# Optimization experiments

Hardware: AMD Instinct MI355X
Metric: run time of the kernel (lower is better)

## Reference

```python
import jax, jax.numpy as jnp
import numpy as np

N_NODES = 100000
N_EDGES = 1600000
IN_DIM = 64
HIDDEN = 64
N_CLASSES = 249


def sage_conv(x, edge_index, W_l, b_l, W_r):
    # PyG SAGEConv with aggr='add': out = lin_l(sum_{j->i} x_j) + lin_r(x_i)
    src, dst = edge_index[0], edge_index[1]
    msgs = x[src]                                   # [E, d] gather
    agg = jax.ops.segment_sum(msgs, dst, num_segments=x.shape[0])  # [N, d]
    return agg @ W_l.T + b_l + x @ W_r.T


def setup_inputs() -> dict:
    key = jax.random.key(0)
    ks = jax.random.split(key, 8)
    x = jax.random.normal(ks[0], (N_NODES, IN_DIM), dtype=jnp.float32)
    edge_index = jax.random.randint(ks[1], (2, N_EDGES), 0, N_NODES, dtype=jnp.int64 if jax.config.jax_enable_x64 else jnp.int32)
    s1 = 1.0 / np.sqrt(IN_DIM)
    s2 = 1.0 / np.sqrt(HIDDEN)
    W1_l = jax.random.uniform(ks[2], (HIDDEN, IN_DIM), jnp.float32, -s1, s1)
    b1_l = jax.random.uniform(ks[3], (HIDDEN,), jnp.float32, -s1, s1)
    W1_r = jax.random.uniform(ks[4], (HIDDEN, IN_DIM), jnp.float32, -s1, s1)
    W2_l = jax.random.uniform(ks[5], (N_CLASSES, HIDDEN), jnp.float32, -s2, s2)
    b2_l = jax.random.uniform(ks[6], (N_CLASSES,), jnp.float32, -s2, s2)
    W2_r = jax.random.uniform(ks[7], (N_CLASSES, HIDDEN), jnp.float32, -s2, s2)
    return {"x": x, "edge_index": edge_index, "W1_l": W1_l, "b1_l": b1_l,
            "W1_r": W1_r, "W2_l": W2_l, "b2_l": b2_l, "W2_r": W2_r}


def reference(x, edge_index, W1_l, b1_l, W1_r, W2_l, b2_l, W2_r):
    h = sage_conv(x, edge_index, W1_l, b1_l, W1_r)
    h = jax.nn.relu(h)
    # dropout p=0.5 is identity at inference (training=False)
    out = sage_conv(h, edge_index, W2_l, b2_l, W2_r)
    return out
```

## Files before the change

### kernel.cpp

```cpp
#include <hip/hip_runtime.h>

#define DIM 64
#define NCLS 249
#define SCAN_CHUNK 1024
#define NCHUNK 192
#define PSHIFT 7
#define PSIZE 128
#define SBITS 17
#define SMASK ((1u << SBITS) - 1)
#define MAXP 1024

typedef unsigned int u32;
typedef unsigned short u16;
using bf16x8 = __attribute__((ext_vector_type(8))) short;
using f32x4  = __attribute__((ext_vector_type(4))) float;

__device__ __forceinline__ u16 f2bf(float f) {
    u32 u = __builtin_bit_cast(u32, f);
    u += 0x7FFFu + ((u >> 16) & 1u);
    return (u16)(u >> 16);
}
__device__ __forceinline__ float bf_lo(u32 u) { return __builtin_bit_cast(float, u << 16); }
__device__ __forceinline__ float bf_hi(u32 u) { return __builtin_bit_cast(float, u & 0xFFFF0000u); }

__global__ __launch_bounds__(256) void bucket_count(const int* __restrict__ dst, int E,
                                                    int chunk_size, int nxp,
                                                    int* __restrict__ bcnt) {
    __shared__ int c[MAXP];
    int t = threadIdx.x;
    for (int i = t; i < nxp; i += 256) c[i] = 0;
    __syncthreads();
    int base = blockIdx.x * chunk_size;
    int end = min(base + chunk_size, E);
    for (int e = base + t; e < end; e += 256) {
        int d = __builtin_nontemporal_load(&dst[e]);
        atomicAdd(&c[d >> PSHIFT], 1);
    }
    __syncthreads();
    for (int i = t; i < nxp; i += 256) bcnt[i * NCHUNK + blockIdx.x] = c[i];
}

__global__ __launch_bounds__(256) void scan_block_sums(const int* __restrict__ cnt, int n,
                                                       int* __restrict__ bsum) {
    __shared__ int sdata[256];
    int b = blockIdx.x, t = threadIdx.x;
    int base = b * SCAN_CHUNK;
    int s = 0;
    for (int i = t; i < SCAN_CHUNK; i += 256) {
        int idx = base + i;
        s += (idx < n) ? cnt[idx] : 0;
    }
    sdata[t] = s;
    __syncthreads();
    for (int off = 128; off > 0; off >>= 1) {
        if (t < off) sdata[t] += sdata[t + off];
        __syncthreads();
    }
    if (t == 0) bsum[b] = sdata[0];
}

__global__ __launch_bounds__(1024) void scan_bsum(int* __restrict__ bsum, int nb) {
    __shared__ int tmp[1024];
    int t = threadIdx.x;
    int v = (t < nb) ? bsum[t] : 0;
    tmp[t] = v;
    __syncthreads();
    for (int off = 1; off < 1024; off <<= 1) {
        int u = (t >= off) ? tmp[t - off] : 0;
        __syncthreads();
        tmp[t] += u;
        __syncthreads();
    }
    if (t < nb) bsum[t] = tmp[t] - v;
}

__global__ __launch_bounds__(256) void scan_final_boff(const int* __restrict__ cnt, int n,
                                                       const int* __restrict__ bsum,
                                                       int* __restrict__ boff, int total) {
    __shared__ int tsum[256];
    int b = blockIdx.x, t = threadIdx.x;
    int base = b * SCAN_CHUNK + t * 4;
    int v[4];
    int s = 0;
#pragma unroll
    for (int i = 0; i < 4; ++i) {
        int id = base + i;
        v[i] = (id < n) ? cnt[id] : 0;
        s += v[i];
    }
    tsum[t] = s;
    __syncthreads();
    for (int off = 1; off < 256; off <<= 1) {
        int u = (t >= off) ? tsum[t - off] : 0;
        __syncthreads();
        tsum[t] += u;
        __syncthreads();
    }
    int run = tsum[t] - s + bsum[b];
#pragma unroll
    for (int i = 0; i < 4; ++i) {
        int id = base + i;
        if (id < n) boff[id] = run;
        run += v[i];
    }
    if (b == 0 && t == 0) boff[n] = total;
}

__global__ __launch_bounds__(256) void bucket_scatter(const int* __restrict__ ei, int E,
                                                      int chunk_size, int nxp,
                                                      const int* __restrict__ boff,
                                                      u32* __restrict__ bucket) {
    __shared__ int cur[MAXP];
    int t = threadIdx.x;
    for (int i = t; i < nxp; i += 256) cur[i] = boff[i * NCHUNK + blockIdx.x];
    __syncthreads();
    int base = blockIdx.x * chunk_size;
    int end = min(base + chunk_size, E);
    for (int e = base + t; e < end; e += 256) {
        int s = __builtin_nontemporal_load(&ei[e]);
        int d = __builtin_nontemporal_load(&ei[E + e]);
        int pos = atomicAdd(&cur[d >> PSHIFT], 1);
        bucket[pos] = ((u32)(d & (PSIZE - 1)) << SBITS) | (u32)s;
    }
}

__global__ __launch_bounds__(256) void sort_bucket(const u32* __restrict__ bucket,
                                                   const int* __restrict__ boff,
                                                   int* __restrict__ nbr,
                                                   int* __restrict__ row_ptr,
                                                   int n, int E) {
    __shared__ int cnt[PSIZE];
    __shared__ int sc[PSIZE];
    __shared__ int cur[PSIZE];
    int t = threadIdx.x;
    int p = blockIdx.x;
    if (t < PSIZE) cnt[t] = 0;
    __syncthreads();
    int beg = boff[p * NCHUNK];
    int end = boff[(p + 1) * NCHUNK];
    for (int i = beg + t; i < end; i += 256)
        atomicAdd(&cnt[bucket[i] >> SBITS], 1);
    __syncthreads();
    if (t < PSIZE) sc[t] = cnt[t];
    __syncthreads();
    for (int off = 1; off < PSIZE; off <<= 1) {
        int v = 0;
        if (t < PSIZE && t >= off) v = sc[t - off];
        __syncthreads();
        if (t < PSIZE) sc[t] += v;
        __syncthreads();
    }
    if (t < PSIZE) {
        int excl = beg + sc[t] - cnt[t];
        cur[t] = excl;
        int node = p * PSIZE + t;
        if (node < n) row_ptr[node] = excl;
    }
    if (p == 0 && t == 0) row_ptr[n] = E;
    __syncthreads();
    for (int i = beg + t; i < end; i += 256) {
        u32 pk = bucket[i];
        int pos = atomicAdd(&cur[pk >> SBITS], 1);
        nbr[pos] = (int)(pk & SMASK);
    }
}

__global__ void prep_all(const float* __restrict__ x, u16* __restrict__ A1, int nx8,
                         const float* __restrict__ W1l, const float* __restrict__ W1r,
                         u16* __restrict__ B1,
                         const float* __restrict__ W2l, const float* __restrict__ W2r,
                         u16* __restrict__ B2) {
    int i = blockIdx.x * 256 + threadIdx.x;
    if (i < nx8) {
        int node = i >> 3, seg = i & 7;
        const float4 v0 = *(const float4*)(x + (size_t)i * 8);
        const float4 v1 = *(const float4*)(x + (size_t)i * 8 + 4);
        uint4 o;
        o.x = (u32)f2bf(v0.x) | ((u32)f2bf(v0.y) << 16);
        o.y = (u32)f2bf(v0.z) | ((u32)f2bf(v0.w) << 16);
        o.z = (u32)f2bf(v1.x) | ((u32)f2bf(v1.y) << 16);
        o.w = (u32)f2bf(v1.z) | ((u32)f2bf(v1.w) << 16);
        *(uint4*)(A1 + (size_t)node * 128 + 64 + seg * 8) = o;
        return;
    }
    int j = i - nx8;
    if (j < 64 * 128) {
        int r = j >> 7, k = j & 127;
        B1[j] = f2bf(k < 64 ? W1l[r * 64 + k] : W1r[r * 64 + k - 64]);
        return;
    }
    j -= 64 * 128;
    if (j < 256 * 128) {
        int r = j >> 7, k = j & 127;
        float v = 0.f;
        if (r < NCLS) v = (k < 64) ? W2l[r * 64 + k] : W2r[r * 64 + k - 64];
        B2[j] = f2bf(v);
    }
}

__global__ __launch_bounds__(256) void pull_bf16(const u16* __restrict__ Asrc,
                                                 const int* __restrict__ row_ptr,
                                                 const int* __restrict__ nbr,
                                                 u16* __restrict__ Adst, int n) {
    int tid = blockIdx.x * 256 + threadIdx.x;
    int node = tid >> 3;
    int q = tid & 7;
    if (node >= n) return;
    int beg = row_ptr[node], end = row_ptr[node + 1];
    float a0 = 0.f, a1 = 0.f, a2 = 0.f, a3 = 0.f, a4 = 0.f, a5 = 0.f, a6 = 0.f, a7 = 0.f;
    for (int j0 = beg; j0 < end; j0 += 8) {
        int myj = j0 + q;
        int smine = (myj < end) ? nbr[myj] : 0;
        int cnt = min(8, end - j0);
#pragma unroll 4
        for (int k = 0; k < cnt; ++k) {
            int s = __shfl(smine, k, 8);
            uint4 v = *(const uint4*)(Asrc + (size_t)s * 128 + 64 + q * 8);
            a0 += bf_lo(v.x); a1 += bf_hi(v.x);
            a2 += bf_lo(v.y); a3 += bf_hi(v.y);
            a4 += bf_lo(v.z); a5 += bf_hi(v.z);
            a6 += bf_lo(v.w); a7 += bf_hi(v.w);
        }
    }
    uint4 o;
    o.x = (u32)f2bf(a0) | ((u32)f2bf(a1) << 16);
    o.y = (u32)f2bf(a2) | ((u32)f2bf(a3) << 16);
    o.z = (u32)f2bf(a4) | ((u32)f2bf(a5) << 16);
    o.w = (u32)f2bf(a6) | ((u32)f2bf(a7) << 16);
    *(uint4*)(Adst + (size_t)node * 128 + q * 8) = o;
}

template<int NT, bool RELU, bool OUT_BF16>
__global__ __launch_bounds__(256) void gemm_kernel(
    const u16* __restrict__ A, const u16* __restrict__ B,
    const float* __restrict__ bias,
    float* __restrict__ outf, u16* __restrict__ outb,
    int n_nodes, int n_cols)
{
    constexpr int KC = (NT == 16) ? 2 : 1;
    constexpr int KW = 128 / KC;
    constexpr int RG = KW / 8;
    constexpr int NR = NT * 16;
    __shared__ uint4 smem[3072];
    uint4* A_lds = smem;
    uint4* B_lds = smem + 1024;

    const int t = threadIdx.x;
    const int node0 = blockIdx.x * 64;

#pragma unroll
    for (int i = 0; i < 4; ++i) {
        int gl = t + 256 * i;
        int r = gl >> 4, g = gl & 15;
        uint4 v = make_uint4(0u, 0u, 0u, 0u);
        int node = node0 + r;
        if (node < n_nodes) v = *(const uint4*)(A + (size_t)node * 128 + g * 8);
        A_lds[r * 16 + (g ^ (r & 7))] = v;
    }

    const int w  = t >> 6;
    const int l  = t & 63;
    const int lm = l & 15;
    const int lg = l >> 4;
    const int arow = w * 16 + lm;
    const int asw  = arow & 7;

    f32x4 acc[NT];
#pragma unroll
    for (int n = 0; n < NT; ++n) acc[n] = f32x4{0.f, 0.f, 0.f, 0.f};

#pragma unroll
    for (int kc = 0; kc < KC; ++kc) {
        __syncthreads();
#pragma unroll
        for (int i = 0; i < (NR * RG) / 256; ++i) {
            int gl = t + 256 * i;
            int r = gl / RG, g = gl % RG;
            uint4 v = *(const uint4*)(B + (size_t)r * 128 + kc * KW + g * 8);
            B_lds[r * RG + (g ^ (r & 7))] = v;
        }
        __syncthreads();
#pragma unroll
        for (int ks = 0; ks < KW / 32; ++ks) {
            int ag = lg + (kc * (KW / 32) + ks) * 4;
            bf16x8 af = __builtin_bit_cast(bf16x8, A_lds[arow * 16 + (ag ^ asw)]);
#pragma unroll
            for (int n = 0; n < NT; ++n) {
                int brow = n * 16 + lm;
                int bg = lg + ks * 4;
                bf16x8 bf = __builtin_bit_cast(bf16x8, B_lds[brow * RG + (bg ^ (brow & 7))]);
                acc[n] = __builtin_amdgcn_mfma_f32_16x16x32_bf16(af, bf, acc[n], 0, 0, 0);
            }
        }
    }

    if (OUT_BF16) {
        const int rbase = w * 16 + lg * 4;
#pragma unroll
        for (int n = 0; n < NT; ++n) {
            int c = n * 16 + lm;
            float bv = (c < n_cols) ? bias[c] : 0.f;
#pragma unroll
            for (int r = 0; r < 4; ++r) {
                int node = node0 + rbase + r;
                if (node < n_nodes && c < n_cols) {
                    float v = acc[n][r] + bv;
                    if (RELU) v = fmaxf(v, 0.f);
                    outb[(size_t)node * 128 + 64 + c] = f2bf(v);
                }
            }
        }
    } else {
        float bc[NT];
#pragma unroll
        for (int n = 0; n < NT; ++n) {
            int c = n * 16 + lm;
            bc[n] = (c < n_cols) ? bias[c] : 0.f;
        }
        float* S = reinterpret_cast<float*>(smem);
        __syncthreads();
#pragma unroll
        for (int rc = 0; rc < 2; ++rc) {
            if (rc) __syncthreads();
            if ((lg >> 1) == rc) {
                int lrow = (lg & 1) * 4;
                float* Sw = S + ((size_t)w * 8 + lrow) * 264;
#pragma unroll
                for (int n = 0; n < NT; ++n) {
#pragma unroll
                    for (int r = 0; r < 4; ++r) {
                        float v = acc[n][r] + bc[n];
                        if (RELU) v = fmaxf(v, 0.f);
                        Sw[r * 264 + n * 16 + lm] = v;
                    }
                }
            }
            __syncthreads();
            const float* Sw = S + (size_t)w * 8 * 264;
#pragma unroll
            for (int row8 = 0; row8 < 8; ++row8) {
                int node = node0 + w * 16 + rc * 8 + row8;
                if (node >= n_nodes) continue;
                float* orow = outf + (size_t)node * (size_t)n_cols;
#pragma unroll
                for (int k = 0; k < 4; ++k) {
                    int c = k * 64 + l;
                    if (c < n_cols) orow[c] = Sw[row8 * 264 + c];
                }
            }
        }
    }
}

extern "C" void kernel_launch(void* const* d_in, const int* in_sizes, int n_in,
                              void* d_out, int out_size, void* d_ws, size_t ws_size,
                              hipStream_t stream) {
    const float* x   = (const float*)d_in[0];
    const int*   ei  = (const int*)d_in[1];
    const float* W1l = (const float*)d_in[2];
    const float* b1  = (const float*)d_in[3];
    const float* W1r = (const float*)d_in[4];
    const float* W2l = (const float*)d_in[5];
    const float* b2  = (const float*)d_in[6];
    const float* W2r = (const float*)d_in[7];
    float* out = (float*)d_out;

    const int N = in_sizes[0] / DIM;
    const int E = in_sizes[1] / 2;
    const int NPAD = ((N + 63) / 64) * 64;
    const int NXP = (N + PSIZE - 1) / PSIZE;
    const int NSC = NXP * NCHUNK;
    const int NB2 = (NSC + SCAN_CHUNK - 1) / SCAN_CHUNK;

    char* wp = (char*)d_ws;
    u16* A1 = (u16*)wp;                 wp += (size_t)NPAD * 128 * 2;
    u16* A2 = (u16*)wp;                 wp += (size_t)NPAD * 128 * 2;
    u16* B1 = (u16*)wp;                 wp += 64 * 128 * 2;
    u16* B2 = (u16*)wp;                 wp += 256 * 128 * 2;
    int* bcnt = (int*)wp;               wp += (size_t)NSC * 4;
    int* boff = (int*)wp;               wp += (size_t)(NSC + 1) * 4;
    int* bsum = (int*)wp;               wp += 1024 * 4;
    int* row_ptr = (int*)wp;            wp += (size_t)(N + 1) * 4;
    u32* bucket = (u32*)wp;             wp += (size_t)E * 4;
    int* nbr = (int*)wp;                wp += (size_t)E * 4;

    const int chunk_size = (E + NCHUNK - 1) / NCHUNK;

    bucket_count<<<NCHUNK, 256, 0, stream>>>(ei + E, E, chunk_size, NXP, bcnt);
    scan_block_sums<<<NB2, 256, 0, stream>>>(bcnt, NSC, bsum);
    scan_bsum<<<1, 1024, 0, stream>>>(bsum, NB2);
    scan_final_boff<<<NB2, 256, 0, stream>>>(bcnt, NSC, bsum, boff, E);
    bucket_scatter<<<NCHUNK, 256, 0, stream>>>(ei, E, chunk_size, NXP, boff, bucket);
    sort_bucket<<<NXP, 256, 0, stream>>>(bucket, boff, nbr, row_ptr, N, E);

    const int prep_items = N * 8 + 64 * 128 + 256 * 128;
    prep_all<<<(prep_items + 255) / 256, 256, 0, stream>>>(x, A1, N * 8,
                                                           W1l, W1r, B1, W2l, W2r, B2);

    const int gemm_blocks = NPAD / 64;

    pull_bf16<<<(N * 8 + 255) / 256, 256, 0, stream>>>(A1, row_ptr, nbr, A1, N);
    gemm_kernel<4, true, true><<<gemm_blocks, 256, 0, stream>>>(A1, B1, b1, nullptr, A2, N, 64);

    pull_bf16<<<(N * 8 + 255) / 256, 256, 0, stream>>>(A2, row_ptr, nbr, A2, N);
    gemm_kernel<16, false, false><<<gemm_blocks, 256, 0, stream>>>(A2, B2, b2, out, nullptr, N, NCLS);
}
```

Before: 203.4 us.

## Fuse neighbor aggregation into GEMM kernels and merge setup kernels

The separate pull_bf16 aggregation kernels are removed, and each GEMM block now gathers and sums neighbor features for its 64 nodes straight into LDS, so the aggregated half of A is never written to or re-read from global memory. The edge bucket count and the bf16 conversion of x and the weights are merged into one launch. The single-block scan_bsum is folded into scan_final_boff, where every block redundantly rescans the block sums. This cuts kernel launches and a global round trip, but the GEMM blocks now absorb irregular gather latency and their occupancy is limited by LDS use, which may reduce latency hiding for the gathers.

New measurement: 265.7 us. +30.7%, slower.

```diff
diff --git a/kernel.cpp b/kernel.cpp
--- a/kernel.cpp
+++ b/kernel.cpp
@@ -23,21 +23,54 @@
 __device__ __forceinline__ float bf_lo(u32 u) { return __builtin_bit_cast(float, u << 16); }
 __device__ __forceinline__ float bf_hi(u32 u) { return __builtin_bit_cast(float, u & 0xFFFF0000u); }
 
-__global__ __launch_bounds__(256) void bucket_count(const int* __restrict__ dst, int E,
-                                                    int chunk_size, int nxp,
-                                                    int* __restrict__ bcnt) {
+__global__ __launch_bounds__(256) void build_kernel(
+    const int* __restrict__ dst, int E, int chunk_size, int nxp,
+    int* __restrict__ bcnt,
+    const float* __restrict__ x, u16* __restrict__ A1, int nx8,
+    const float* __restrict__ W1l, const float* __restrict__ W1r, u16* __restrict__ B1,
+    const float* __restrict__ W2l, const float* __restrict__ W2r, u16* __restrict__ B2)
+{
     __shared__ int c[MAXP];
     int t = threadIdx.x;
-    for (int i = t; i < nxp; i += 256) c[i] = 0;
-    __syncthreads();
-    int base = blockIdx.x * chunk_size;
-    int end = min(base + chunk_size, E);
-    for (int e = base + t; e < end; e += 256) {
-        int d = __builtin_nontemporal_load(&dst[e]);
-        atomicAdd(&c[d >> PSHIFT], 1);
-    }
-    __syncthreads();
-    for (int i = t; i < nxp; i += 256) bcnt[i * NCHUNK + blockIdx.x] = c[i];
+    if (blockIdx.x < NCHUNK) {
+        for (int i = t; i < nxp; i += 256) c[i] = 0;
+        __syncthreads();
+        int base = blockIdx.x * chunk_size;
+        int end = min(base + chunk_size, E);
+        for (int e = base + t; e < end; e += 256) {
+            int d = __builtin_nontemporal_load(&dst[e]);
+            atomicAdd(&c[d >> PSHIFT], 1);
+        }
+        __syncthreads();
+        for (int i = t; i < nxp; i += 256) bcnt[i * NCHUNK + blockIdx.x] = c[i];
+        return;
+    }
+    int i = (blockIdx.x - NCHUNK) * 256 + t;
+    if (i < nx8) {
+        int node = i >> 3, seg = i & 7;
+        const float4 v0 = *(const float4*)(x + (size_t)i * 8);
+        const float4 v1 = *(const float4*)(x + (size_t)i * 8 + 4);
+        uint4 o;
+        o.x = (u32)f2bf(v0.x) | ((u32)f2bf(v0.y) << 16);
+        o.y = (u32)f2bf(v0.z) | ((u32)f2bf(v0.w) << 16);
+        o.z = (u32)f2bf(v1.x) | ((u32)f2bf(v1.y) << 16);
+        o.w = (u32)f2bf(v1.z) | ((u32)f2bf(v1.w) << 16);
+        *(uint4*)(A1 + (size_t)node * 128 + 64 + seg * 8) = o;
+        return;
+    }
+    int j = i - nx8;
+    if (j < 64 * 128) {
+        int r = j >> 7, k = j & 127;
+        B1[j] = f2bf(k < 64 ? W1l[r * 64 + k] : W1r[r * 64 + k - 64]);
+        return;
+    }
+    j -= 64 * 128;
+    if (j < 256 * 128) {
+        int r = j >> 7, k = j & 127;
+        float v = 0.f;
+        if (r < NCLS) v = (k < 64) ? W2l[r * 64 + k] : W2r[r * 64 + k - 64];
+        B2[j] = f2bf(v);
+    }
 }
 
 __global__ __launch_bounds__(256) void scan_block_sums(const int* __restrict__ cnt, int n,
@@ -59,26 +92,22 @@
     if (t == 0) bsum[b] = sdata[0];
 }
 
-__global__ __launch_bounds__(1024) void scan_bsum(int* __restrict__ bsum, int nb) {
-    __shared__ int tmp[1024];
-    int t = threadIdx.x;
-    int v = (t < nb) ? bsum[t] : 0;
-    tmp[t] = v;
-    __syncthreads();
-    for (int off = 1; off < 1024; off <<= 1) {
-        int u = (t >= off) ? tmp[t - off] : 0;
-        __syncthreads();
-        tmp[t] += u;
-        __syncthreads();
-    }
-    if (t < nb) bsum[t] = tmp[t] - v;
-}
-
 __global__ __launch_bounds__(256) void scan_final_boff(const int* __restrict__ cnt, int n,
-                                                       const int* __restrict__ bsum,
+                                                       const int* __restrict__ bsum_raw, int nb,
                                                        int* __restrict__ boff, int total) {
+    __shared__ int bpre[256];
     __shared__ int tsum[256];
     int b = blockIdx.x, t = threadIdx.x;
+    int bv = (t < nb) ? bsum_raw[t] : 0;
+    bpre[t] = bv;
+    __syncthreads();
+    for (int off = 1; off < 256; off <<= 1) {
+        int u = (t >= off) ? bpre[t - off] : 0;
+        __syncthreads();
+        bpre[t] += u;
+        __syncthreads();
+    }
+    int block_base = (b == 0) ? 0 : bpre[b - 1];
     int base = b * SCAN_CHUNK + t * 4;
     int v[4];
     int s = 0;
@@ -96,7 +125,7 @@
         tsum[t] += u;
         __syncthreads();
     }
-    int run = tsum[t] - s + bsum[b];
+    int run = tsum[t] - s + block_base;
 #pragma unroll
     for (int i = 0; i < 4; ++i) {
         int id = base + i;
@@ -165,75 +194,11 @@
     }
 }
 
-__global__ void prep_all(const float* __restrict__ x, u16* __restrict__ A1, int nx8,
-                         const float* __restrict__ W1l, const float* __restrict__ W1r,
-                         u16* __restrict__ B1,
-                         const float* __restrict__ W2l, const float* __restrict__ W2r,
-                         u16* __restrict__ B2) {
-    int i = blockIdx.x * 256 + threadIdx.x;
-    if (i < nx8) {
-        int node = i >> 3, seg = i & 7;
-        const float4 v0 = *(const float4*)(x + (size_t)i * 8);
-        const float4 v1 = *(const float4*)(x + (size_t)i * 8 + 4);
-        uint4 o;
-        o.x = (u32)f2bf(v0.x) | ((u32)f2bf(v0.y) << 16);
-        o.y = (u32)f2bf(v0.z) | ((u32)f2bf(v0.w) << 16);
-        o.z = (u32)f2bf(v1.x) | ((u32)f2bf(v1.y) << 16);
-        o.w = (u32)f2bf(v1.z) | ((u32)f2bf(v1.w) << 16);
-        *(uint4*)(A1 + (size_t)node * 128 + 64 + seg * 8) = o;
-        return;
-    }
-    int j = i - nx8;
-    if (j < 64 * 128) {
-        int r = j >> 7, k = j & 127;
-        B1[j] = f2bf(k < 64 ? W1l[r * 64 + k] : W1r[r * 64 + k - 64]);
-        return;
-    }
-    j -= 64 * 128;
-    if (j < 256 * 128) {
-        int r = j >> 7, k = j & 127;
-        float v = 0.f;
-        if (r < NCLS) v = (k < 64) ? W2l[r * 64 + k] : W2r[r * 64 + k - 64];
-        B2[j] = f2bf(v);
-    }
-}
-
-__global__ __launch_bounds__(256) void pull_bf16(const u16* __restrict__ Asrc,
-                                                 const int* __restrict__ row_ptr,
-                                                 const int* __restrict__ nbr,
-                                                 u16* __restrict__ Adst, int n) {
-    int tid = blockIdx.x * 256 + threadIdx.x;
-    int node = tid >> 3;
-    int q = tid & 7;
-    if (node >= n) return;
-    int beg = row_ptr[node], end = row_ptr[node + 1];
-    float a0 = 0.f, a1 = 0.f, a2 = 0.f, a3 = 0.f, a4 = 0.f, a5 = 0.f, a6 = 0.f, a7 = 0.f;
-    for (int j0 = beg; j0 < end; j0 += 8) {
-        int myj = j0 + q;
-        int smine = (myj < end) ? nbr[myj] : 0;
-        int cnt = min(8, end - j0);
-#pragma unroll 4
-        for (int k = 0; k < cnt; ++k) {
-            int s = __shfl(smine, k, 8);
-            uint4 v = *(const uint4*)(Asrc + (size_t)s * 128 + 64 + q * 8);
-            a0 += bf_lo(v.x); a1 += bf_hi(v.x);
-            a2 += bf_lo(v.y); a3 += bf_hi(v.y);
-            a4 += bf_lo(v.z); a5 += bf_hi(v.z);
-            a6 += bf_lo(v.w); a7 += bf_hi(v.w);
-        }
-    }
-    uint4 o;
-    o.x = (u32)f2bf(a0) | ((u32)f2bf(a1) << 16);
-    o.y = (u32)f2bf(a2) | ((u32)f2bf(a3) << 16);
-    o.z = (u32)f2bf(a4) | ((u32)f2bf(a5) << 16);
-    o.w = (u32)f2bf(a6) | ((u32)f2bf(a7) << 16);
-    *(uint4*)(Adst + (size_t)node * 128 + q * 8) = o;
-}
-
 template<int NT, bool RELU, bool OUT_BF16>
-__global__ __launch_bounds__(256) void gemm_kernel(
+__global__ __launch_bounds__(256) void gemm_fused(
     const u16* __restrict__ A, const u16* __restrict__ B,
     const float* __restrict__ bias,
+    const int* __restrict__ row_ptr, const int* __restrict__ nbr,
     float* __restrict__ outf, u16* __restrict__ outb,
     int n_nodes, int n_cols)
 {
@@ -247,15 +212,48 @@
 
     const int t = threadIdx.x;
     const int node0 = blockIdx.x * 64;
-
-#pragma unroll
-    for (int i = 0; i < 4; ++i) {
+    const int q = t & 7;
+
+#pragma unroll
+    for (int i = 0; i < 2; ++i) {
         int gl = t + 256 * i;
-        int r = gl >> 4, g = gl & 15;
+        int r = gl >> 3;
+        int g = 8 + (gl & 7);
         uint4 v = make_uint4(0u, 0u, 0u, 0u);
         int node = node0 + r;
         if (node < n_nodes) v = *(const uint4*)(A + (size_t)node * 128 + g * 8);
         A_lds[r * 16 + (g ^ (r & 7))] = v;
+    }
+
+#pragma unroll
+    for (int pass = 0; pass < 2; ++pass) {
+        int nl = (t >> 3) + pass * 32;
+        int node = node0 + nl;
+        float a0 = 0.f, a1 = 0.f, a2 = 0.f, a3 = 0.f,
+              a4 = 0.f, a5 = 0.f, a6 = 0.f, a7 = 0.f;
+        if (node < n_nodes) {
+            int beg = row_ptr[node], end = row_ptr[node + 1];
+            for (int j0 = beg; j0 < end; j0 += 8) {
+                int myj = j0 + q;
+                int smine = (myj < end) ? nbr[myj] : 0;
+                int cnt = min(8, end - j0);
+#pragma unroll 4
+                for (int k = 0; k < cnt; ++k) {
+                    int s = __shfl(smine, k, 8);
+                    uint4 v = *(const uint4*)(A + (size_t)s * 128 + 64 + q * 8);
+                    a0 += bf_lo(v.x); a1 += bf_hi(v.x);
+                    a2 += bf_lo(v.y); a3 += bf_hi(v.y);
+                    a4 += bf_lo(v.z); a5 += bf_hi(v.z);
+                    a6 += bf_lo(v.w); a7 += bf_hi(v.w);
+                }
+            }
+        }
+        uint4 o;
+        o.x = (u32)f2bf(a0) | ((u32)f2bf(a1) << 16);
+        o.y = (u32)f2bf(a2) | ((u32)f2bf(a3) << 16);
+        o.z = (u32)f2bf(a4) | ((u32)f2bf(a5) << 16);
+        o.w = (u32)f2bf(a6) | ((u32)f2bf(a7) << 16);
+        A_lds[nl * 16 + (q ^ (nl & 7))] = o;
     }
 
     const int w  = t >> 6;
@@ -385,23 +383,24 @@
     int* nbr = (int*)wp;                wp += (size_t)E * 4;
 
     const int chunk_size = (E + NCHUNK - 1) / NCHUNK;
-
-    bucket_count<<<NCHUNK, 256, 0, stream>>>(ei + E, E, chunk_size, NXP, bcnt);
+    const int nx8 = N * 8;
+    const int prep_items = nx8 + 64 * 128 + 256 * 128;
+    const int prep_blocks = (prep_items + 255) / 256;
+
+    build_kernel<<<NCHUNK + prep_blocks, 256, 0, stream>>>(
+        ei + E, E, chunk_size, NXP, bcnt, x, A1, nx8, W1l, W1r, B1, W2l, W2r, B2);
+
     scan_block_sums<<<NB2, 256, 0, stream>>>(bcnt, NSC, bsum);
-    scan_bsum<<<1, 1024, 0, stream>>>(bsum, NB2);
-    scan_final_boff<<<NB2, 256, 0, stream>>>(bcnt, NSC, bsum, boff, E);
+    scan_final_boff<<<NB2, 256, 0, stream>>>(bcnt, NSC, bsum, NB2, boff, E);
+
     bucket_scatter<<<NCHUNK, 256, 0, stream>>>(ei, E, chunk_size, NXP, boff, bucket);
     sort_bucket<<<NXP, 256, 0, stream>>>(bucket, boff, nbr, row_ptr, N, E);
 
-    const int prep_items = N * 8 + 64 * 128 + 256 * 128;
-    prep_all<<<(prep_items + 255) / 256, 256, 0, stream>>>(x, A1, N * 8,
-                                                           W1l, W1r, B1, W2l, W2r, B2);
-
     const int gemm_blocks = NPAD / 64;
 
-    pull_bf16<<<(N * 8 + 255) / 256, 256, 0, stream>>>(A1, row_ptr, nbr, A1, N);
-    gemm_kernel<4, true, true><<<gemm_blocks, 256, 0, stream>>>(A1, B1, b1, nullptr, A2, N, 64);
-
-    pull_bf16<<<(N * 8 + 255) / 256, 256, 0, stream>>>(A2, row_ptr, nbr, A2, N);
-    gemm_kernel<16, false, false><<<gemm_blocks, 256, 0, stream>>>(A2, B2, b2, out, nullptr, N, NCLS);
-}
+    gemm_fused<4, true, true><<<gemm_blocks, 256, 0, stream>>>(
+        A1, B1, b1, row_ptr, nbr, nullptr, A2, N, 64);
+
+    gemm_fused<16, false, false><<<gemm_blocks, 256, 0, stream>>>(
+        A2, B2, b2, row_ptr, nbr, out, nullptr, N, NCLS);
+}
```
